# Optimization experiments

Hardware: AMD Instinct MI355X
Metric: run time of the kernel (lower is better)

The kernel has to match this reference:

```python
import jax, jax.numpy as jnp
import numpy as np
from jax import lax

B, T_ENC, IN, H, V, EMB = 128, 512, 2, 256, 29, 8


def _gru_cell(x_t, h, Wih, Whh, bih, bhh):
    # PyTorch GRU cell, gate order (r, z, n)
    gi = x_t @ Wih.T + bih            # [B, 3H]
    gh = h @ Whh.T + bhh              # [B, 3H]
    ir, iz, inn = jnp.split(gi, 3, axis=-1)
    hr, hz, hn = jnp.split(gh, 3, axis=-1)
    r = jax.nn.sigmoid(ir + hr)
    z = jax.nn.sigmoid(iz + hz)
    n = jnp.tanh(inn + r * hn)
    return (1.0 - z) * n + z * h


def _gru_scan(xs, Wih, Whh, bih, bhh, reverse):
    # xs: [B, T, D] -> outputs [B, T, H], final hidden [B, H]
    h0 = jnp.zeros((xs.shape[0], Whh.shape[-1]), xs.dtype)
    def step(h, x_t):
        h = _gru_cell(x_t, h, Wih, Whh, bih, bhh)
        return h, h
    hT, ys = lax.scan(step, h0, jnp.swapaxes(xs, 0, 1), reverse=reverse)
    return jnp.swapaxes(ys, 0, 1), hT


def _forward(x, target_seq, eWih0, eWhh0, ebih0, ebhh0, eWih1, eWhh1, ebih1, ebhh1,
             e2d_W, e2d_b, dWih0, dWih1, dWhh, dbih, dbhh, q_W, q_b, out_W, out_b, emb):
    # ---- bidirectional 2-layer GRU encoder ----
    yf0, hf0 = _gru_scan(x, eWih0[0], eWhh0[0], ebih0[0], ebhh0[0], False)
    yb0, hb0 = _gru_scan(x, eWih0[1], eWhh0[1], ebih0[1], ebhh0[1], True)
    y0 = jnp.concatenate([yf0, yb0], axis=-1)          # [B, T, 2H]
    yf1, hf1 = _gru_scan(y0, eWih1[0], eWhh1[0], ebih1[0], ebhh1[0], False)
    yb1, hb1 = _gru_scan(y0, eWih1[1], eWhh1[1], ebih1[1], ebhh1[1], True)
    y1 = jnp.concatenate([yf1, yb1], axis=-1)          # [B, T, 2H]
    enc_out = y1 @ e2d_W.T + e2d_b                     # [B, T, H]
    # hidden.reshape(L, 2, B, H).sum(dim=1): fwd + bwd per layer
    h0c = hf0 + hb0
    h1c = hf1 + hb1

    max_steps = target_seq.shape[1] - 1
    init_tok = target_seq[:, 0]

    def dec_step(carry, _):
        h0, h1, tok = carry
        e = emb[tok]                                   # [B, EMB]
        h0 = _gru_cell(e, h0, dWih0, dWhh[0], dbih[0], dbhh[0])
        h1 = _gru_cell(h0, h1, dWih1, dWhh[1], dbih[1], dbhh[1])
        q = h1 @ q_W.T + q_b                           # [B, H]
        scores = jnp.einsum('bte,be->bt', enc_out, q)  # [B, T]
        w = jax.nn.softmax(scores, axis=1)
        ctx = jnp.einsum('bt,bte->be', w, enc_out)     # [B, H]
        logits = (h1 + ctx) @ out_W.T + out_b          # [B, V] (dropout is identity in eval)
        tok = jnp.argmax(logits, axis=-1)
        return (h0, h1, tok), logits

    (h0c, h1c, _), logits = lax.scan(dec_step, (h0c, h1c, init_tok), None, length=max_steps)
    logits = jnp.swapaxes(logits, 0, 1)                # [B, max_steps, V]
    hidden = jnp.stack([h0c, h1c], axis=0)             # [L, B, H]
    return logits, hidden


def setup_inputs() -> dict:
    key = jax.random.key(0)
    ks = jax.random.split(key, 24)
    def p(k, *shape):
        return jax.random.normal(k, shape, jnp.float32) * 0.05
    return {
        'x': jax.random.normal(ks[0], (B, T_ENC, IN), jnp.float32),
        'target_seq': jax.random.randint(ks[1], (B, 64), 0, V),
        'eWih0': p(ks[2], 2, 3 * H, IN),
        'eWhh0': p(ks[3], 2, 3 * H, H),
        'ebih0': p(ks[4], 2, 3 * H),
        'ebhh0': p(ks[5], 2, 3 * H),
        'eWih1': p(ks[6], 2, 3 * H, 2 * H),
        'eWhh1': p(ks[7], 2, 3 * H, H),
        'ebih1': p(ks[8], 2, 3 * H),
        'ebhh1': p(ks[9], 2, 3 * H),
        'e2d_W': p(ks[10], H, 2 * H),
        'e2d_b': p(ks[11], H),
        'dWih0': p(ks[12], 3 * H, EMB),
        'dWih1': p(ks[13], 3 * H, H),
        'dWhh': p(ks[14], 2, 3 * H, H),
        'dbih': p(ks[15], 2, 3 * H),
        'dbhh': p(ks[16], 2, 3 * H),
        'q_W': p(ks[17], H, H),
        'q_b': p(ks[18], H),
        'out_W': p(ks[19], V, H),
        'out_b': p(ks[20], V),
        'emb': p(ks[21], V, EMB),
    }


def reference(x, target_seq, eWih0, eWhh0, ebih0, ebhh0, eWih1, eWhh1, ebih1, ebhh1,
              e2d_W, e2d_b, dWih0, dWih1, dWhh, dbih, dbhh, q_W, q_b, out_W, out_b, emb):
    return _forward(x, target_seq, eWih0, eWhh0, ebih0, ebhh0, eWih1, eWhh1, ebih1, ebhh1,
                    e2d_W, e2d_b, dWih0, dWih1, dWhh, dbih, dbhh, q_W, q_b, out_W, out_b, emb)
```

## Files before the change

kernel.cpp:

```cpp
#include <hip/hip_runtime.h>
#include <hip/hip_bf16.h>
#include <hip/hip_fp16.h>
#include <stdint.h>

#define BB 128
#define TT 512
#define HH 256
#define VV 29
#define NSTEP 63
#define BT (BB*TT)
#define CHUNK 64

typedef _Float16 f16;
typedef _Float16 f16x2 __attribute__((ext_vector_type(2)));
typedef _Float16 f16x8 __attribute__((ext_vector_type(8)));
typedef float f32x4 __attribute__((ext_vector_type(4)));

static __device__ __forceinline__ float fdot2u(uint32_t a, uint32_t b, float c) {
  return __builtin_amdgcn_fdot2(__builtin_bit_cast(f16x2, a),
                                __builtin_bit_cast(f16x2, b), c, false);
}
static __device__ __forceinline__ float sigm_(float x) {
  return 1.0f / (1.0f + __expf(-x));
}

__global__ void k_cvt(const float* __restrict__ s, f16* __restrict__ d, int n) {
  int i = blockIdx.x * 256 + threadIdx.x;
  if (i < n) d[i] = (f16)s[i];
}

template<int LAYER>
__global__ __launch_bounds__(512, 2)
void k_scan(const float* __restrict__ x,
            const f16* __restrict__ gi,
            const uint32_t* __restrict__ whh,
            const float* __restrict__ wih0,
            const float* __restrict__ bih,
            const float* __restrict__ bhh,
            f16* __restrict__ y,
            float* __restrict__ hstate,
            int t0, int nsteps)
{
  const int wg = blockIdx.x, b = wg >> 1, dir = wg & 1;
  const int tid = threadIdx.x, pair = tid >> 1, half = tid & 1;
  __shared__ __align__(16) uint4 hv4[32];

  uint4 w0[16], w1[16], w2[16];
  {
    const uint32_t* wp = whh + (size_t)dir * 768 * 128;
    const uint4* r0 = (const uint4*)(wp + (size_t)pair * 128 + half * 64);
    const uint4* r1 = (const uint4*)(wp + (size_t)(pair + 256) * 128 + half * 64);
    const uint4* r2 = (const uint4*)(wp + (size_t)(pair + 512) * 128 + half * 64);
#pragma unroll
    for (int i = 0; i < 16; i++) { w0[i] = r0[i]; w1[i] = r1[i]; w2[i] = r2[i]; }
  }
  const float bh0 = bhh[dir * 768 + pair];
  const float bh1 = bhh[dir * 768 + pair + 256];
  const float bh2 = bhh[dir * 768 + pair + 512];
  float bi0 = 0, bi1 = 0, bi2 = 0;
  float wi00 = 0, wi01 = 0, wi10 = 0, wi11 = 0, wi20 = 0, wi21 = 0;
  if (LAYER == 0) {
    bi0 = bih[dir * 768 + pair];
    bi1 = bih[dir * 768 + pair + 256];
    bi2 = bih[dir * 768 + pair + 512];
    wi00 = wih0[(dir * 768 + pair) * 2 + 0];
    wi01 = wih0[(dir * 768 + pair) * 2 + 1];
    wi10 = wih0[(dir * 768 + pair + 256) * 2 + 0];
    wi11 = wih0[(dir * 768 + pair + 256) * 2 + 1];
    wi20 = wih0[(dir * 768 + pair + 512) * 2 + 0];
    wi21 = wih0[(dir * 768 + pair + 512) * 2 + 1];
  }
  float* hs = hstate + ((size_t)dir * BB + b) * 256;
  float hreg = hs[pair];
  if (tid < 128) {
    f16x2 p2; p2[0] = (f16)hs[2 * tid]; p2[1] = (f16)hs[2 * tid + 1];
    ((uint32_t*)hv4)[tid] = __builtin_bit_cast(uint32_t, p2);
  }
  __syncthreads();

  const uint4* hw = hv4 + half * 16;
  for (int s = 0; s < nsteps; ++s) {
    const int t = dir ? (TT - 1 - t0 - s) : (t0 + s);
    float gr, gz, gn;
    if (LAYER == 0) {
      float x0 = x[((size_t)b * TT + t) * 2 + 0];
      float x1 = x[((size_t)b * TT + t) * 2 + 1];
      gr = wi00 * x0 + wi01 * x1 + bi0;
      gz = wi10 * x0 + wi11 * x1 + bi1;
      gn = wi20 * x0 + wi21 * x1 + bi2;
    } else {
      const f16* g = gi + ((size_t)b * nsteps + s) * 1536 + dir * 768 + pair;
      gr = (float)g[0]; gz = (float)g[256]; gn = (float)g[512];
    }
    float a0 = 0.f, a1 = 0.f, a2 = 0.f;
#pragma unroll
    for (int j = 0; j < 16; ++j) {
      uint4 hh = hw[j];
      a0 = fdot2u(w0[j].x, hh.x, a0); a0 = fdot2u(w0[j].y, hh.y, a0);
      a0 = fdot2u(w0[j].z, hh.z, a0); a0 = fdot2u(w0[j].w, hh.w, a0);
      a1 = fdot2u(w1[j].x, hh.x, a1); a1 = fdot2u(w1[j].y, hh.y, a1);
      a1 = fdot2u(w1[j].z, hh.z, a1); a1 = fdot2u(w1[j].w, hh.w, a1);
      a2 = fdot2u(w2[j].x, hh.x, a2); a2 = fdot2u(w2[j].y, hh.y, a2);
      a2 = fdot2u(w2[j].z, hh.z, a2); a2 = fdot2u(w2[j].w, hh.w, a2);
    }
    a0 += __shfl_xor(a0, 1);
    a1 += __shfl_xor(a1, 1);
    a2 += __shfl_xor(a2, 1);

    float r = sigm_(gr + a0 + bh0);
    float z = sigm_(gz + a1 + bh1);
    float n = tanhf(gn + r * (a2 + bh2));
    float hn = (1.0f - z) * n + z * hreg;
    hreg = hn;
    if (half == 0) y[((size_t)b * TT + t) * 512 + dir * 256 + pair] = (f16)hn;
    __syncthreads();
    if (half == 0) ((f16*)hv4)[pair] = (f16)hn;
    __syncthreads();
  }
  if (half == 0) hs[pair] = hreg;
}

__global__ __launch_bounds__(256)
void k_gemm(const f16* __restrict__ A, const f16* __restrict__ Bt,
            f16* __restrict__ C, const float* __restrict__ bias,
            int K, int shift, long bstride, int inner, int ldc, int coloff)
{
  const int m0 = blockIdx.x * 64, n0 = blockIdx.y * 64;
  const int tid = threadIdx.x, lane = tid & 63, wv = tid >> 6;
  __shared__ __align__(16) f16 As[64 * 40];
  __shared__ __align__(16) f16 Bs[64 * 40];
  f32x4 acc[4] = {{0,0,0,0},{0,0,0,0},{0,0,0,0},{0,0,0,0}};
  const int lrow = tid >> 2, lseg = tid & 3;
  const int ml = lane & 15, quad = lane >> 4;
  const int r = m0 + lrow;
  const f16* arow = A + (long)(r >> shift) * bstride
                      + (long)(r & ((1 << shift) - 1)) * inner;
  const f16* brow = Bt + (size_t)(n0 + lrow) * K;
  for (int k0 = 0; k0 < K; k0 += 32) {
    uint4 av = *(const uint4*)(arow + k0 + lseg * 8);
    uint4 bv = *(const uint4*)(brow + k0 + lseg * 8);
    __syncthreads();
    *(uint4*)(As + lrow * 40 + lseg * 8) = av;
    *(uint4*)(Bs + lrow * 40 + lseg * 8) = bv;
    __syncthreads();
    f16x8 af = *(const f16x8*)(As + (wv * 16 + ml) * 40 + quad * 8);
#pragma unroll
    for (int ns = 0; ns < 4; ++ns) {
      f16x8 bf = *(const f16x8*)(Bs + (ns * 16 + ml) * 40 + quad * 8);
      acc[ns] = __builtin_amdgcn_mfma_f32_16x16x32_f16(af, bf, acc[ns], 0, 0, 0);
    }
  }
#pragma unroll
  for (int ns = 0; ns < 4; ++ns) {
#pragma unroll
    for (int rr = 0; rr < 4; ++rr) {
      int row = m0 + wv * 16 + quad * 4 + rr;
      int col = n0 + ns * 16 + ml;
      float v = acc[ns][rr];
      if (bias) v += bias[col];
      C[(size_t)row * ldc + coloff + col] = (f16)v;
    }
  }
}

static __device__ __forceinline__ float dot256(const uint4* __restrict__ w,
                                               const uint4* __restrict__ h) {
  float g = 0.f;
#pragma unroll 8
  for (int j = 0; j < 32; ++j) {
    uint4 a = w[j], b = h[j];
    g = fdot2u(a.x, b.x, g); g = fdot2u(a.y, b.y, g);
    g = fdot2u(a.z, b.z, g); g = fdot2u(a.w, b.w, g);
  }
  return g;
}
static __device__ __forceinline__ float dot128(const uint4* __restrict__ w,
                                               const uint4* __restrict__ h) {
  float g = 0.f;
#pragma unroll 8
  for (int j = 0; j < 16; ++j) {
    uint4 a = w[j], b = h[j];
    g = fdot2u(a.x, b.x, g); g = fdot2u(a.y, b.y, g);
    g = fdot2u(a.z, b.z, g); g = fdot2u(a.w, b.w, g);
  }
  return g;
}
static __device__ __forceinline__ float edot(uint4 w, const float* e) {
  f16x2 a = __builtin_bit_cast(f16x2, w.x);
  f16x2 b = __builtin_bit_cast(f16x2, w.y);
  f16x2 c = __builtin_bit_cast(f16x2, w.z);
  f16x2 d = __builtin_bit_cast(f16x2, w.w);
  return (float)a[0]*e[0] + (float)a[1]*e[1] + (float)b[0]*e[2] + (float)b[1]*e[3]
       + (float)c[0]*e[4] + (float)c[1]*e[5] + (float)d[0]*e[6] + (float)d[1]*e[7];
}

__global__ __launch_bounds__(768, 3)
void k_decoder(const f16* __restrict__ dwhh,
               const f16* __restrict__ dwih1,
               const f16* __restrict__ dwih0,
               const f16* __restrict__ qw,
               const f16* __restrict__ outw,
               const f16* __restrict__ enc,
               const float* __restrict__ dbih,
               const float* __restrict__ dbhh,
               const float* __restrict__ qb, const float* __restrict__ outb,
               const float* __restrict__ emb,
               const float* __restrict__ hs0, const float* __restrict__ hs1,
               const int* __restrict__ tseq,
               float* __restrict__ out)
{
  const int b = blockIdx.x, tid = threadIdx.x;
  __shared__ __align__(16) f16 h0sh[256], h1sh[256], qsh[256];
  __shared__ float h1f[256];
  __shared__ float g0sh[768], g1sh[768], gi0n[256], gi1sh[768];
  __shared__ float qpart[2][256];
  __shared__ float sc[512];
  __shared__ float redm[12], redl[12];
  __shared__ __align__(16) float cpart[4][256];
  __shared__ __align__(16) float hc[256];
  __shared__ float lg[32];
  __shared__ float e8[8];
  __shared__ int toksh;

  if (tid < 256) {
    h0sh[tid] = (f16)(hs0[b * 256 + tid] + hs0[32768 + b * 256 + tid]);
    h1sh[tid] = (f16)(hs1[b * 256 + tid] + hs1[32768 + b * 256 + tid]);
  }
  if (tid == 0) {
    int tk = tseq[b * 64]; toksh = tk;
    for (int k = 0; k < 8; ++k) e8[k] = emb[tk * 8 + k];
  }
  __syncthreads();

  const int wvi = tid >> 6;

  for (int s = 0; s < NSTEP; ++s) {
    {
      const uint4* wA = (const uint4*)(dwhh + (size_t)tid * 256);
      const uint4* wB = (const uint4*)(dwhh + (size_t)(768 + tid) * 256);
      const uint4* h0q = (const uint4*)h0sh;
      const uint4* h1q = (const uint4*)h1sh;
      float gA = dbhh[tid], gB = dbhh[768 + tid];
#pragma unroll 8
      for (int j = 0; j < 32; ++j) {
        uint4 a = wA[j], ha = h0q[j];
        uint4 c = wB[j], hb = h1q[j];
        gA = fdot2u(a.x, ha.x, gA); gA = fdot2u(a.y, ha.y, gA);
        gA = fdot2u(a.z, ha.z, gA); gA = fdot2u(a.w, ha.w, gA);
        gB = fdot2u(c.x, hb.x, gB); gB = fdot2u(c.y, hb.y, gB);
        gB = fdot2u(c.z, hb.z, gB); gB = fdot2u(c.w, hb.w, gB);
      }
      uint4 wi = *(const uint4*)(dwih0 + (size_t)tid * 8);
      float gi = dbih[tid] + edot(wi, e8);
      if (tid < 512) g0sh[tid] = gA + gi;
      else { g0sh[tid] = gA; gi0n[tid - 512] = gi; }
      g1sh[tid] = gB;
    }
    __syncthreads();

    if (tid < 256) {
      float r = sigm_(g0sh[tid]);
      float z = sigm_(g0sh[tid + 256]);
      float n = tanhf(gi0n[tid] + r * g0sh[tid + 512]);
      float hp = (float)h0sh[tid];
      h0sh[tid] = (f16)((1.f - z) * n + z * hp);
    }
    __syncthreads();

    gi1sh[tid] = dbih[768 + tid] +
                 dot256((const uint4*)(dwih1 + (size_t)tid * 256), (const uint4*)h0sh);
    __syncthreads();

    if (tid < 256) {
      float r = sigm_(gi1sh[tid] + g1sh[tid]);
      float z = sigm_(gi1sh[tid + 256] + g1sh[tid + 256]);
      float n = tanhf(gi1sh[tid + 512] + r * g1sh[tid + 512]);
      float hp = (float)h1sh[tid];
      float hn = (1.f - z) * n + z * hp;
      h1f[tid] = hn;
      h1sh[tid] = (f16)hn;
    }
    __syncthreads();

    if (tid < 512) {
      int row = tid & 255, kh = tid >> 8;
      qpart[kh][row] = dot128((const uint4*)(qw + (size_t)row * 256 + kh * 128),
                              (const uint4*)h1sh + kh * 16);
    }
    __syncthreads();
    if (tid < 256) qsh[tid] = (f16)(qpart[0][tid] + qpart[1][tid] + qb[tid]);
    __syncthreads();

    if (tid < 512)
      sc[tid] = dot256((const uint4*)(enc + ((size_t)b * 512 + tid) * 256),
                       (const uint4*)qsh);
    __syncthreads();

    float v = (tid < 512) ? sc[tid] : -1e30f;
    float mloc = v;
#pragma unroll
    for (int off = 32; off; off >>= 1) mloc = fmaxf(mloc, __shfl_xor(mloc, off));
    if ((tid & 63) == 0) redm[wvi] = mloc;
    __syncthreads();
    float m = redm[0];
#pragma unroll
    for (int i = 1; i < 12; ++i) m = fmaxf(m, redm[i]);
    float e = 0.f;
    if (tid < 512) { e = __expf(v - m); sc[tid] = e; }
    float lloc = e;
#pragma unroll
    for (int off = 32; off; off >>= 1) lloc += __shfl_xor(lloc, off);
    if ((tid & 63) == 0) redl[wvi] = lloc;
    __syncthreads();
    float l = redl[0];
#pragma unroll
    for (int i = 1; i < 12; ++i) l += redl[i];

    if (tid < 512) {
      const int c2 = tid & 127, seg = tid >> 7;
      const uint32_t* eb = (const uint32_t*)enc + (((size_t)b * 512 + seg * 128) * 128) + c2;
      const float* wsc = sc + seg * 128;
      float c0 = 0.f, c1 = 0.f;
#pragma unroll 8
      for (int i = 0; i < 128; ++i) {
        uint32_t vv = eb[(size_t)i * 128];
        float wgt = wsc[i];
        f16x2 h2 = __builtin_bit_cast(f16x2, vv);
        c0 += wgt * (float)h2[0];
        c1 += wgt * (float)h2[1];
      }
      ((float2*)cpart[seg])[c2] = float2{c0, c1};
    }
    __syncthreads();
    if (tid < 256)
      hc[tid] = (cpart[0][tid] + cpart[1][tid] + cpart[2][tid] + cpart[3][tid]) / l
                + h1f[tid];
    __syncthreads();

    if (tid < VV * 8) {
      const int vv = tid >> 3, kseg = tid & 7;
      float acc = 0.f;
      const uint4* ow = (const uint4*)(outw + (size_t)vv * 256 + kseg * 32);
      const float4* hv = (const float4*)(hc + kseg * 32);
#pragma unroll
      for (int j = 0; j < 4; ++j) {
        uint4 wq = ow[j];
        float4 ha = hv[2 * j], hb = hv[2 * j + 1];
        f16x2 p0 = __builtin_bit_cast(f16x2, wq.x);
        f16x2 p1 = __builtin_bit_cast(f16x2, wq.y);
        f16x2 p2 = __builtin_bit_cast(f16x2, wq.z);
        f16x2 p3 = __builtin_bit_cast(f16x2, wq.w);
        acc += (float)p0[0]*ha.x + (float)p0[1]*ha.y + (float)p1[0]*ha.z + (float)p1[1]*ha.w;
        acc += (float)p2[0]*hb.x + (float)p2[1]*hb.y + (float)p3[0]*hb.z + (float)p3[1]*hb.w;
      }
      acc += __shfl_xor(acc, 1);
      acc += __shfl_xor(acc, 2);
      acc += __shfl_xor(acc, 4);
      if (kseg == 0) {
        float lv = acc + outb[vv];
        lg[vv] = lv;
        out[((size_t)b * NSTEP + s) * VV + vv] = lv;
      }
    }
    __syncthreads();
    if (tid == 0) {
      int best = 0; float bv = lg[0];
      for (int v2 = 1; v2 < VV; ++v2) if (lg[v2] > bv) { bv = lg[v2]; best = v2; }
      toksh = best;
      for (int k = 0; k < 8; ++k) e8[k] = emb[best * 8 + k];
    }
    __syncthreads();
  }

  if (tid < 256) {
    out[233856 + b * 256 + tid] = (float)h0sh[tid];
    out[233856 + 32768 + b * 256 + tid] = (float)h1sh[tid];
  }
}

extern "C" void kernel_launch(void* const* d_in, const int* in_sizes, int n_in,
                              void* d_out, int out_size, void* d_ws, size_t ws_size,
                              hipStream_t stream) {
  (void)in_sizes; (void)n_in; (void)out_size; (void)ws_size;
  const float* x     = (const float*)d_in[0];
  const int*   tseq  = (const int*)d_in[1];
  const float* eWih0 = (const float*)d_in[2];
  const float* eWhh0 = (const float*)d_in[3];
  const float* ebih0 = (const float*)d_in[4];
  const float* ebhh0 = (const float*)d_in[5];
  const float* eWih1 = (const float*)d_in[6];
  const float* eWhh1 = (const float*)d_in[7];
  const float* ebih1 = (const float*)d_in[8];
  const float* ebhh1 = (const float*)d_in[9];
  const float* e2dW  = (const float*)d_in[10];
  const float* e2db  = (const float*)d_in[11];
  const float* dWih0 = (const float*)d_in[12];
  const float* dWih1 = (const float*)d_in[13];
  const float* dWhh  = (const float*)d_in[14];
  const float* dbih  = (const float*)d_in[15];
  const float* dbhh  = (const float*)d_in[16];
  const float* qW    = (const float*)d_in[17];
  const float* qb    = (const float*)d_in[18];
  const float* outW  = (const float*)d_in[19];
  const float* outb  = (const float*)d_in[20];
  const float* emb   = (const float*)d_in[21];

  uint8_t* ws = (uint8_t*)d_ws;
  size_t o = 0;
  auto take = [&](size_t bytes) -> void* {
    void* p = ws + o;
    o += (bytes + 255) & ~(size_t)255;
    return p;
  };
  f16* whh0_16  = (f16*)take((size_t)2 * 768 * 256 * 2);
  f16* whh1_16  = (f16*)take((size_t)2 * 768 * 256 * 2);
  f16* wih1_16  = (f16*)take((size_t)2 * 768 * 512 * 2);
  f16* e2d_16   = (f16*)take((size_t)256 * 512 * 2);
  f16* qw_16    = (f16*)take((size_t)256 * 256 * 2);
  f16* outw_16  = (f16*)take((size_t)29 * 256 * 2);
  f16* dwih0_16 = (f16*)take((size_t)768 * 8 * 2);
  f16* dwih1_16 = (f16*)take((size_t)768 * 256 * 2);
  f16* dwhh_16  = (f16*)take((size_t)2 * 768 * 256 * 2);
  f16* y0   = (f16*)take((size_t)BT * 512 * 2);
  f16* y1   = (f16*)take((size_t)BT * 512 * 2);
  f16* gi   = (f16*)take((size_t)BB * CHUNK * 1536 * 2);
  float* hs0 = (float*)take((size_t)2 * BB * 256 * 4);
  float* hs1 = (float*)take((size_t)2 * BB * 256 * 4);
  f16* enc = y0;

  hipMemsetAsync(hs0, 0, (size_t)2 * BB * 256 * 4, stream);
  hipMemsetAsync(hs1, 0, (size_t)2 * BB * 256 * 4, stream);

  auto cvt = [&](const float* s, f16* d, int n) {
    k_cvt<<<(n + 255) / 256, 256, 0, stream>>>(s, d, n);
  };
  cvt(eWhh0, whh0_16, 2 * 768 * 256);
  cvt(eWhh1, whh1_16, 2 * 768 * 256);
  cvt(eWih1, wih1_16, 2 * 768 * 512);
  cvt(e2dW,  e2d_16,  256 * 512);
  cvt(qW,    qw_16,   256 * 256);
  cvt(outW,  outw_16, 29 * 256);
  cvt(dWih0, dwih0_16, 768 * 8);
  cvt(dWih1, dwih1_16, 768 * 256);
  cvt(dWhh,  dwhh_16, 2 * 768 * 256);

  k_scan<0><<<256, 512, 0, stream>>>(x, nullptr, (const uint32_t*)whh0_16,
                                     eWih0, ebih0, ebhh0, y0, hs0, 0, TT);

  const long BSTR = (long)TT * 512;
  for (int c = 0; c < TT / CHUNK; ++c) {
    const int t0 = c * CHUNK;
    k_gemm<<<dim3(BB * CHUNK / 64, 12), 256, 0, stream>>>(
        y0 + (size_t)t0 * 512, wih1_16, gi, ebih1,
        512, 6, BSTR, 512, 1536, 0);
    k_gemm<<<dim3(BB * CHUNK / 64, 12), 256, 0, stream>>>(
        y0 + (size_t)(TT - 1 - t0) * 512, wih1_16 + (size_t)768 * 512, gi, ebih1 + 768,
        512, 6, BSTR, -512, 1536, 768);
    k_scan<1><<<256, 512, 0, stream>>>(nullptr, gi, (const uint32_t*)whh1_16,
                                       nullptr, nullptr, ebhh1, y1, hs1, t0, CHUNK);
  }

  k_gemm<<<dim3(BT / 64, 4), 256, 0, stream>>>(y1, e2d_16, enc, e2db,
                                               512, 30, 0, 512, 256, 0);

  k_decoder<<<128, 768, 0, stream>>>(dwhh_16, dwih1_16, dwih0_16, qw_16, outw_16,
                                     enc, dbih, dbhh, qb, outb, emb,
                                     hs0, hs1, tseq, (float*)d_out);
}
```

Measured before the change: 5.640 ms.

## Fold query projection into encoder outputs to remove per-step q GEMV

```diff
diff --git a/kernel.cpp b/kernel.cpp
--- a/kernel.cpp
+++ b/kernel.cpp
@@ -15,6 +15,7 @@
 typedef _Float16 f16x2 __attribute__((ext_vector_type(2)));
 typedef _Float16 f16x8 __attribute__((ext_vector_type(8)));
 typedef float f32x4 __attribute__((ext_vector_type(4)));
+typedef unsigned int u32x4 __attribute__((ext_vector_type(4)));
 
 static __device__ __forceinline__ float fdot2u(uint32_t a, uint32_t b, float c) {
   return __builtin_amdgcn_fdot2(__builtin_bit_cast(f16x2, a),
@@ -27,6 +28,33 @@
 __global__ void k_cvt(const float* __restrict__ s, f16* __restrict__ d, int n) {
   int i = blockIdx.x * 256 + threadIdx.x;
   if (i < n) d[i] = (f16)s[i];
+}
+__global__ void k_qwt(const float* __restrict__ s, f16* __restrict__ d) {
+  int i = blockIdx.x * 256 + threadIdx.x;
+  int n = i >> 8, e = i & 255;
+  d[n * 256 + e] = (f16)s[e * 256 + n];
+}
+__global__ void k_sb(const f16* __restrict__ enc, const float* __restrict__ qb,
+                     float* __restrict__ sb) {
+  __shared__ float qbs[256];
+  int tid = threadIdx.x;
+  qbs[tid] = qb[tid];
+  __syncthreads();
+  int i = blockIdx.x * 256 + tid;
+  const uint4* e = (const uint4*)(enc + (size_t)i * 256);
+  float acc = 0.f;
+#pragma unroll 8
+  for (int j = 0; j < 32; ++j) {
+    uint4 v = e[j];
+    f16x2 p0 = __builtin_bit_cast(f16x2, v.x);
+    f16x2 p1 = __builtin_bit_cast(f16x2, v.y);
+    f16x2 p2 = __builtin_bit_cast(f16x2, v.z);
+    f16x2 p3 = __builtin_bit_cast(f16x2, v.w);
+    const float* q = qbs + j * 8;
+    acc += (float)p0[0]*q[0] + (float)p0[1]*q[1] + (float)p1[0]*q[2] + (float)p1[1]*q[3]
+         + (float)p2[0]*q[4] + (float)p2[1]*q[5] + (float)p3[0]*q[6] + (float)p3[1]*q[7];
+  }
+  sb[i] = acc;
 }
 
 template<int LAYER>
@@ -174,17 +202,6 @@
   }
   return g;
 }
-static __device__ __forceinline__ float dot128(const uint4* __restrict__ w,
-                                               const uint4* __restrict__ h) {
-  float g = 0.f;
-#pragma unroll 8
-  for (int j = 0; j < 16; ++j) {
-    uint4 a = w[j], b = h[j];
-    g = fdot2u(a.x, b.x, g); g = fdot2u(a.y, b.y, g);
-    g = fdot2u(a.z, b.z, g); g = fdot2u(a.w, b.w, g);
-  }
-  return g;
-}
 static __device__ __forceinline__ float edot(uint4 w, const float* e) {
   f16x2 a = __builtin_bit_cast(f16x2, w.x);
   f16x2 b = __builtin_bit_cast(f16x2, w.y);
@@ -198,22 +215,22 @@
 void k_decoder(const f16* __restrict__ dwhh,
                const f16* __restrict__ dwih1,
                const f16* __restrict__ dwih0,
-               const f16* __restrict__ qw,
                const f16* __restrict__ outw,
                const f16* __restrict__ enc,
+               const f16* __restrict__ EP,
+               const float* __restrict__ SB,
                const float* __restrict__ dbih,
                const float* __restrict__ dbhh,
-               const float* __restrict__ qb, const float* __restrict__ outb,
+               const float* __restrict__ outb,
                const float* __restrict__ emb,
                const float* __restrict__ hs0, const float* __restrict__ hs1,
                const int* __restrict__ tseq,
                float* __restrict__ out)
 {
   const int b = blockIdx.x, tid = threadIdx.x;
-  __shared__ __align__(16) f16 h0sh[256], h1sh[256], qsh[256];
+  __shared__ __align__(16) f16 h0sh[256], h1sh[256];
   __shared__ float h1f[256];
   __shared__ float g0sh[768], g1sh[768], gi0n[256], gi1sh[768];
-  __shared__ float qpart[2][256];
   __shared__ float sc[512];
   __shared__ float redm[12], redl[12];
   __shared__ __align__(16) float cpart[4][256];
@@ -232,7 +249,7 @@
   }
   __syncthreads();
 
-  const int wvi = tid >> 6;
+  const int wvi = tid >> 6, lane = tid & 63;
 
   for (int s = 0; s < NSTEP; ++s) {
     {
@@ -282,25 +299,36 @@
     }
     __syncthreads();
 
-    if (tid < 512) {
-      int row = tid & 255, kh = tid >> 8;
-      qpart[kh][row] = dot128((const uint4*)(qw + (size_t)row * 256 + kh * 128),
-                              (const uint4*)h1sh + kh * 16);
-    }
-    __syncthreads();
-    if (tid < 256) qsh[tid] = (f16)(qpart[0][tid] + qpart[1][tid] + qb[tid]);
-    __syncthreads();
-
-    if (tid < 512)
-      sc[tid] = dot256((const uint4*)(enc + ((size_t)b * 512 + tid) * 256),
-                       (const uint4*)qsh);
+    {
+      const int seg = lane & 7, rsub = lane >> 3;
+      const uint4* h1q = (const uint4*)h1sh;
+#pragma unroll
+      for (int sweep = 0; sweep < 6; ++sweep) {
+        int r = sweep * 96 + wvi * 8 + rsub;
+        if (r < 512) {
+          const u32x4* ep = (const u32x4*)(EP + ((size_t)b * 512 + r) * 256);
+          float p = 0.f;
+#pragma unroll
+          for (int j = 0; j < 4; ++j) {
+            u32x4 a = __builtin_nontemporal_load(ep + j * 8 + seg);
+            uint4 h = h1q[j * 8 + seg];
+            p = fdot2u(a[0], h.x, p); p = fdot2u(a[1], h.y, p);
+            p = fdot2u(a[2], h.z, p); p = fdot2u(a[3], h.w, p);
+          }
+          p += __shfl_xor(p, 1);
+          p += __shfl_xor(p, 2);
+          p += __shfl_xor(p, 4);
+          if (seg == 0) sc[r] = p + SB[b * 512 + r];
+        }
+      }
+    }
     __syncthreads();
 
     float v = (tid < 512) ? sc[tid] : -1e30f;
     float mloc = v;
 #pragma unroll
     for (int off = 32; off; off >>= 1) mloc = fmaxf(mloc, __shfl_xor(mloc, off));
-    if ((tid & 63) == 0) redm[wvi] = mloc;
+    if (lane == 0) redm[wvi] = mloc;
     __syncthreads();
     float m = redm[0];
 #pragma unroll
@@ -310,7 +338,7 @@
     float lloc = e;
 #pragma unroll
     for (int off = 32; off; off >>= 1) lloc += __shfl_xor(lloc, off);
-    if ((tid & 63) == 0) redl[wvi] = lloc;
+    if (lane == 0) redl[wvi] = lloc;
     __syncthreads();
     float l = redl[0];
 #pragma unroll
@@ -323,7 +351,7 @@
       float c0 = 0.f, c1 = 0.f;
 #pragma unroll 8
       for (int i = 0; i < 128; ++i) {
-        uint32_t vv = eb[(size_t)i * 128];
+        uint32_t vv = __builtin_nontemporal_load(eb + (size_t)i * 128);
         float wgt = wsc[i];
         f16x2 h2 = __builtin_bit_cast(f16x2, vv);
         c0 += wgt * (float)h2[0];
@@ -416,7 +444,7 @@
   f16* whh1_16  = (f16*)take((size_t)2 * 768 * 256 * 2);
   f16* wih1_16  = (f16*)take((size_t)2 * 768 * 512 * 2);
   f16* e2d_16   = (f16*)take((size_t)256 * 512 * 2);
-  f16* qw_16    = (f16*)take((size_t)256 * 256 * 2);
+  f16* qwt_16   = (f16*)take((size_t)256 * 256 * 2);
   f16* outw_16  = (f16*)take((size_t)29 * 256 * 2);
   f16* dwih0_16 = (f16*)take((size_t)768 * 8 * 2);
   f16* dwih1_16 = (f16*)take((size_t)768 * 256 * 2);
@@ -426,7 +454,9 @@
   f16* gi   = (f16*)take((size_t)BB * CHUNK * 1536 * 2);
   float* hs0 = (float*)take((size_t)2 * BB * 256 * 4);
   float* hs1 = (float*)take((size_t)2 * BB * 256 * 4);
+  float* SBp = (float*)take((size_t)BT * 4);
   f16* enc = y0;
+  f16* EP  = y1;
 
   hipMemsetAsync(hs0, 0, (size_t)2 * BB * 256 * 4, stream);
   hipMemsetAsync(hs1, 0, (size_t)2 * BB * 256 * 4, stream);
@@ -438,11 +468,11 @@
   cvt(eWhh1, whh1_16, 2 * 768 * 256);
   cvt(eWih1, wih1_16, 2 * 768 * 512);
   cvt(e2dW,  e2d_16,  256 * 512);
-  cvt(qW,    qw_16,   256 * 256);
   cvt(outW,  outw_16, 29 * 256);
   cvt(dWih0, dwih0_16, 768 * 8);
   cvt(dWih1, dwih1_16, 768 * 256);
   cvt(dWhh,  dwhh_16, 2 * 768 * 256);
+  k_qwt<<<256, 256, 0, stream>>>(qW, qwt_16);
 
   k_scan<0><<<256, 512, 0, stream>>>(x, nullptr, (const uint32_t*)whh0_16,
                                      eWih0, ebih0, ebhh0, y0, hs0, 0, TT);
@@ -462,8 +492,11 @@
 
   k_gemm<<<dim3(BT / 64, 4), 256, 0, stream>>>(y1, e2d_16, enc, e2db,
                                                512, 30, 0, 512, 256, 0);
-
-  k_decoder<<<128, 768, 0, stream>>>(dwhh_16, dwih1_16, dwih0_16, qw_16, outw_16,
-                                     enc, dbih, dbhh, qb, outb, emb,
+  k_gemm<<<dim3(BT / 64, 4), 256, 0, stream>>>(enc, qwt_16, EP, nullptr,
+                                               256, 30, 0, 256, 256, 0);
+  k_sb<<<256, 256, 0, stream>>>(enc, qb, SBp);
+
+  k_decoder<<<128, 768, 0, stream>>>(dwhh_16, dwih1_16, dwih0_16, outw_16,
+                                     enc, EP, SBp, dbih, dbhh, outb, emb,
                                      hs0, hs1, tseq, (float*)d_out);
 }
```

Measured after the change: 8.030 ms. 42.4% more time.

## Split decoder batch across two workgroups with LDS-resident encoder halves

Applied to the files above, without the earlier changes.

```diff
diff --git a/kernel.cpp b/kernel.cpp
--- a/kernel.cpp
+++ b/kernel.cpp
@@ -10,6 +10,7 @@
 #define NSTEP 63
 #define BT (BB*TT)
 #define CHUNK 64
+#define EROW 264
 
 typedef _Float16 f16;
 typedef _Float16 f16x2 __attribute__((ext_vector_type(2)));
@@ -194,7 +195,7 @@
        + (float)c[0]*e[4] + (float)c[1]*e[5] + (float)d[0]*e[6] + (float)d[1]*e[7];
 }
 
-__global__ __launch_bounds__(768, 3)
+__global__ __launch_bounds__(768, 1)
 void k_decoder(const f16* __restrict__ dwhh,
                const f16* __restrict__ dwih1,
                const f16* __restrict__ dwih0,
@@ -207,21 +208,30 @@
                const float* __restrict__ emb,
                const float* __restrict__ hs0, const float* __restrict__ hs1,
                const int* __restrict__ tseq,
+               float* __restrict__ xbuf,
+               int* __restrict__ flag,
                float* __restrict__ out)
 {
-  const int b = blockIdx.x, tid = threadIdx.x;
+  extern __shared__ __align__(16) f16 encsh[];
+  const int wg = blockIdx.x, b = wg >> 1, h = wg & 1;
+  const int tid = threadIdx.x;
   __shared__ __align__(16) f16 h0sh[256], h1sh[256], qsh[256];
   __shared__ float h1f[256];
   __shared__ float g0sh[768], g1sh[768], gi0n[256], gi1sh[768];
   __shared__ float qpart[2][256];
-  __shared__ float sc[512];
+  __shared__ float sc[256];
   __shared__ float redm[12], redl[12];
-  __shared__ __align__(16) float cpart[4][256];
+  __shared__ __align__(16) float cpart[2][256];
   __shared__ __align__(16) float hc[256];
   __shared__ float lg[32];
   __shared__ float e8[8];
   __shared__ int toksh;
 
+  for (int i = tid; i < 256 * 32; i += 768) {
+    const int r = i >> 5, seg = i & 31;
+    *(uint4*)(encsh + (size_t)r * EROW + seg * 8) =
+        *(const uint4*)(enc + (((size_t)b * 512 + h * 256 + r) * 256) + seg * 8);
+  }
   if (tid < 256) {
     h0sh[tid] = (f16)(hs0[b * 256 + tid] + hs0[32768 + b * 256 + tid]);
     h1sh[tid] = (f16)(hs1[b * 256 + tid] + hs1[32768 + b * 256 + tid]);
@@ -232,7 +242,12 @@
   }
   __syncthreads();
 
-  const int wvi = tid >> 6;
+  const int wvi = tid >> 6, lane = tid & 63;
+  float* xw_base = xbuf + ((size_t)(b * 2 + h)) * 272;
+  const float* xr_base = xbuf + ((size_t)(b * 2 + (h ^ 1))) * 272;
+  int* myflag = flag + b * 2 + h;
+  int* pflag = flag + b * 2 + (h ^ 1);
+  (void)myflag;
 
   for (int s = 0; s < NSTEP; ++s) {
     {
@@ -291,26 +306,25 @@
     if (tid < 256) qsh[tid] = (f16)(qpart[0][tid] + qpart[1][tid] + qb[tid]);
     __syncthreads();
 
-    if (tid < 512)
-      sc[tid] = dot256((const uint4*)(enc + ((size_t)b * 512 + tid) * 256),
-                       (const uint4*)qsh);
-    __syncthreads();
-
-    float v = (tid < 512) ? sc[tid] : -1e30f;
+    if (tid < 256)
+      sc[tid] = dot256((const uint4*)(encsh + (size_t)tid * EROW), (const uint4*)qsh);
+    __syncthreads();
+
+    float v = (tid < 256) ? sc[tid] : -1e30f;
     float mloc = v;
 #pragma unroll
     for (int off = 32; off; off >>= 1) mloc = fmaxf(mloc, __shfl_xor(mloc, off));
-    if ((tid & 63) == 0) redm[wvi] = mloc;
+    if (lane == 0) redm[wvi] = mloc;
     __syncthreads();
     float m = redm[0];
 #pragma unroll
     for (int i = 1; i < 12; ++i) m = fmaxf(m, redm[i]);
     float e = 0.f;
-    if (tid < 512) { e = __expf(v - m); sc[tid] = e; }
+    if (tid < 256) { e = __expf(v - m); sc[tid] = e; }
     float lloc = e;
 #pragma unroll
     for (int off = 32; off; off >>= 1) lloc += __shfl_xor(lloc, off);
-    if ((tid & 63) == 0) redl[wvi] = lloc;
+    if (lane == 0) redl[wvi] = lloc;
     __syncthreads();
     float l = redl[0];
 #pragma unroll
@@ -318,23 +332,51 @@
 
     if (tid < 512) {
       const int c2 = tid & 127, seg = tid >> 7;
-      const uint32_t* eb = (const uint32_t*)enc + (((size_t)b * 512 + seg * 128) * 128) + c2;
+      const f16* eb = encsh + (size_t)seg * 128 * EROW + c2 * 2;
       const float* wsc = sc + seg * 128;
       float c0 = 0.f, c1 = 0.f;
 #pragma unroll 8
       for (int i = 0; i < 128; ++i) {
-        uint32_t vv = eb[(size_t)i * 128];
+        f16x2 h2 = *(const f16x2*)(eb + (size_t)i * EROW);
         float wgt = wsc[i];
-        f16x2 h2 = __builtin_bit_cast(f16x2, vv);
         c0 += wgt * (float)h2[0];
         c1 += wgt * (float)h2[1];
       }
       ((float2*)cpart[seg])[c2] = float2{c0, c1};
     }
     __syncthreads();
-    if (tid < 256)
-      hc[tid] = (cpart[0][tid] + cpart[1][tid] + cpart[2][tid] + cpart[3][tid]) / l
-                + h1f[tid];
+
+    {
+      float* xw = xw_base + (s & 1) * 256 * 272;
+      const float* xr = xr_base + (s & 1) * 256 * 272;
+      if (tid < 256) {
+        float cp = cpart[0][tid] + cpart[1][tid];
+        hc[tid] = cp;
+        __hip_atomic_store(xw + tid, cp, __ATOMIC_RELAXED, __HIP_MEMORY_SCOPE_AGENT);
+      }
+      if (tid == 0) {
+        __hip_atomic_store(xw + 256, m, __ATOMIC_RELAXED, __HIP_MEMORY_SCOPE_AGENT);
+        __hip_atomic_store(xw + 257, l, __ATOMIC_RELAXED, __HIP_MEMORY_SCOPE_AGENT);
+      }
+      __syncthreads();
+      if (tid == 0) {
+        __threadfence();
+        __hip_atomic_store(myflag, s + 1, __ATOMIC_RELEASE, __HIP_MEMORY_SCOPE_AGENT);
+        while (__hip_atomic_load(pflag, __ATOMIC_ACQUIRE, __HIP_MEMORY_SCOPE_AGENT) < s + 1) {
+          __builtin_amdgcn_s_sleep(4);
+        }
+      }
+      __syncthreads();
+      if (tid < 256) {
+        float cp_p = __hip_atomic_load(xr + tid, __ATOMIC_RELAXED, __HIP_MEMORY_SCOPE_AGENT);
+        float m_p  = __hip_atomic_load(xr + 256, __ATOMIC_RELAXED, __HIP_MEMORY_SCOPE_AGENT);
+        float l_p  = __hip_atomic_load(xr + 257, __ATOMIC_RELAXED, __HIP_MEMORY_SCOPE_AGENT);
+        float M = fmaxf(m, m_p);
+        float wme = __expf(m - M), wpp = __expf(m_p - M);
+        float L = l * wme + l_p * wpp;
+        hc[tid] = (hc[tid] * wme + cp_p * wpp) / L + h1f[tid];
+      }
+    }
     __syncthreads();
 
     if (tid < VV * 8) {
@@ -359,7 +401,7 @@
       if (kseg == 0) {
         float lv = acc + outb[vv];
         lg[vv] = lv;
-        out[((size_t)b * NSTEP + s) * VV + vv] = lv;
+        if (h == 0) out[((size_t)b * NSTEP + s) * VV + vv] = lv;
       }
     }
     __syncthreads();
@@ -372,7 +414,7 @@
     __syncthreads();
   }
 
-  if (tid < 256) {
+  if (h == 0 && tid < 256) {
     out[233856 + b * 256 + tid] = (float)h0sh[tid];
     out[233856 + 32768 + b * 256 + tid] = (float)h1sh[tid];
   }
@@ -426,10 +468,13 @@
   f16* gi   = (f16*)take((size_t)BB * CHUNK * 1536 * 2);
   float* hs0 = (float*)take((size_t)2 * BB * 256 * 4);
   float* hs1 = (float*)take((size_t)2 * BB * 256 * 4);
+  float* xbuf = (float*)take((size_t)2 * 256 * 272 * 4);
+  int* flags  = (int*)take((size_t)256 * 4);
   f16* enc = y0;
 
   hipMemsetAsync(hs0, 0, (size_t)2 * BB * 256 * 4, stream);
   hipMemsetAsync(hs1, 0, (size_t)2 * BB * 256 * 4, stream);
+  hipMemsetAsync(flags, 0, (size_t)256 * 4, stream);
 
   auto cvt = [&](const float* s, f16* d, int n) {
     k_cvt<<<(n + 255) / 256, 256, 0, stream>>>(s, d, n);
@@ -463,7 +508,11 @@
   k_gemm<<<dim3(BT / 64, 4), 256, 0, stream>>>(y1, e2d_16, enc, e2db,
                                                512, 30, 0, 512, 256, 0);
 
-  k_decoder<<<128, 768, 0, stream>>>(dwhh_16, dwih1_16, dwih0_16, qw_16, outw_16,
-                                     enc, dbih, dbhh, qb, outb, emb,
-                                     hs0, hs1, tseq, (float*)d_out);
-}
+  const size_t dynlds = (size_t)256 * EROW * 2;
+  hipFuncSetAttribute((const void*)k_decoder,
+                      hipFuncAttributeMaxDynamicSharedMemorySize, (int)dynlds);
+  k_decoder<<<256, 768, dynlds, stream>>>(dwhh_16, dwih1_16, dwih0_16, qw_16,
+                                          outw_16, enc, dbih, dbhh, qb, outb, emb,
+                                          hs0, hs1, tseq, xbuf, flags,
+                                          (float*)d_out);
+}
```

After: 6.499 ms. 1.15x slower.
